# Kernel optimization log

Measured on AMD Instinct MI355X. Metric: run time of the kernel, lower is better.

The kernel has to match this reference:

```python
import jax, jax.numpy as jnp
import numpy as np

N_NODES = 100000
N_EDGES = 1600000
IN_C, HID_C, OUT_C = 128, 128, 64


def gcn_conv(x, src, dst, ew, W, b, n_nodes):
    """PyG GCNConv: symmetric-normalized aggregation with added self-loops.

    out = D^{-1/2} (A + I) D^{-1/2} (x @ W) + b,  D = deg(A+I)
    """
    h = x @ W  # [N, C_out]
    # degree at target nodes, including self-loop weight of 1
    deg = jax.ops.segment_sum(ew, dst, num_segments=n_nodes) + 1.0  # [N]
    dinv = jnp.where(deg > 0, jax.lax.rsqrt(deg), 0.0)
    norm = dinv[src] * ew * dinv[dst]  # [E]
    # gather-scale-scatter over edges + self-loop term (norm_ii = 1/deg_i)
    agg = jax.ops.segment_sum(h[src] * norm[:, None], dst, num_segments=n_nodes)
    agg = agg + h * (dinv * dinv)[:, None]
    return agg + b


def setup_inputs() -> dict:
    key = jax.random.key(0)
    ks = jax.random.split(key, 7)
    x = jax.random.normal(ks[0], (N_NODES, IN_C), dtype=jnp.float32)
    edge_index = jax.random.randint(ks[1], (2, N_EDGES), 0, N_NODES, dtype=jnp.int32)
    edge_weight = jax.random.uniform(ks[2], (N_EDGES,), dtype=jnp.float32)
    W1 = jax.random.normal(ks[3], (IN_C, HID_C), dtype=jnp.float32) / np.sqrt(IN_C)
    b1 = jnp.zeros((HID_C,), dtype=jnp.float32)
    W2 = jax.random.normal(ks[4], (HID_C, OUT_C), dtype=jnp.float32) / np.sqrt(HID_C)
    b2 = jnp.zeros((OUT_C,), dtype=jnp.float32)
    return {"x": x, "edge_index": edge_index, "edge_weight": edge_weight,
            "W1": W1, "b1": b1, "W2": W2, "b2": b2}


def reference(x, edge_index, edge_weight, W1, b1, W2, b2):
    src, dst = edge_index[0], edge_index[1]
    n = x.shape[0]
    h = gcn_conv(x, src, dst, edge_weight, W1, b1, n)
    h = jax.nn.relu(h)
    out = gcn_conv(h, src, dst, edge_weight, W2, b2, n)
    return out
```

## Files before the change

### kernel.cpp

```cpp
#include <hip/hip_runtime.h>


#define N_NODES 100000
#define CHUNK   2048
#define NBUCK   196
#define BSHIFT  9
#define BNODES  512
#define CAP     10240

typedef __attribute__((ext_vector_type(8))) short bf16x8;
typedef __attribute__((ext_vector_type(4))) float f32x4;

__device__ __forceinline__ unsigned bf16r(float f) {
    unsigned u = __float_as_uint(f);
    return (u + 0x7fffu + ((u >> 16) & 1u)) >> 16;
}
__device__ __forceinline__ float bf_lo(unsigned u) { return __uint_as_float(u << 16); }
__device__ __forceinline__ float bf_hi(unsigned u) { return __uint_as_float(u & 0xffff0000u); }

__device__ __forceinline__ void fma8(float* a, uint4 u, float w) {
    a[0] = fmaf(bf_lo(u.x), w, a[0]); a[1] = fmaf(bf_hi(u.x), w, a[1]);
    a[2] = fmaf(bf_lo(u.y), w, a[2]); a[3] = fmaf(bf_hi(u.y), w, a[3]);
    a[4] = fmaf(bf_lo(u.z), w, a[4]); a[5] = fmaf(bf_hi(u.z), w, a[5]);
    a[6] = fmaf(bf_lo(u.w), w, a[6]); a[7] = fmaf(bf_hi(u.w), w, a[7]);
}


__global__ __launch_bounds__(256) void a2F_kernel(
    const int* __restrict__ src, const int* __restrict__ dst,
    const float* __restrict__ ew, const float* __restrict__ W1,
    const float* __restrict__ W2, unsigned* __restrict__ Wt1,
    unsigned* __restrict__ Wt2, int* __restrict__ bucketCur,
    uint2* __restrict__ csrTmp, int E)
{
    __shared__ int hist[256], sc[256], exc[256], lcur[256], basel[256];
    __shared__ uint2 ent[CHUNK];
    __shared__ unsigned short bof[CHUNK];

    int t = threadIdx.x;
    if (blockIdx.x == 0) {
        for (int f = t; f < 128 * 64; f += 256) {
            int c = f % 128, j = f / 128;
            Wt1[c * 64 + j] = bf16r(W1[(size_t)(2 * j) * 128 + c]) |
                              (bf16r(W1[(size_t)(2 * j + 1) * 128 + c]) << 16);
        }
        return;
    }
    if (blockIdx.x == 1) {
        for (int f = t; f < 64 * 64; f += 256) {
            int c = f % 64, j = f / 64;
            Wt2[c * 64 + j] = bf16r(W2[(size_t)(2 * j) * 64 + c]) |
                              (bf16r(W2[(size_t)(2 * j + 1) * 64 + c]) << 16);
        }
        return;
    }
    int blk = blockIdx.x - 2;
    hist[t] = 0; lcur[t] = 0;
    __syncthreads();

    int e0 = blk * CHUNK;
    int nv = min(CHUNK, E - e0);
    int dv[CHUNK / 256]; int sv[CHUNK / 256]; unsigned wv[CHUNK / 256];
#pragma unroll
    for (int j = 0; j < CHUNK / 256; ++j) {
        int idx = t + j * 256;
        if (idx < nv) {
            int e = e0 + idx;
            dv[j] = dst[e]; sv[j] = src[e]; wv[j] = __float_as_uint(ew[e]);
            atomicAdd(&hist[dv[j] >> BSHIFT], 1);
        } else dv[j] = -1;
    }
    __syncthreads();
    int hv = hist[t];
    sc[t] = hv;
    __syncthreads();
#pragma unroll
    for (int off = 1; off < 256; off <<= 1) {
        int a = (t >= off) ? sc[t - off] : 0;
        __syncthreads();
        sc[t] += a;
        __syncthreads();
    }
    exc[t] = sc[t] - hv;
    basel[t] = (hv > 0) ? atomicAdd(&bucketCur[t], hv) : 0;
    __syncthreads();
#pragma unroll
    for (int j = 0; j < CHUNK / 256; ++j) {
        if (dv[j] >= 0) {
            int b  = dv[j] >> BSHIFT;
            int dl = dv[j] & (BNODES - 1);
            int p  = exc[b] + atomicAdd(&lcur[b], 1);
            ent[p] = make_uint2(((unsigned)dl << 17) | (unsigned)sv[j], wv[j]);
            bof[p] = (unsigned short)b;
        }
    }
    __syncthreads();
#pragma unroll
    for (int j = 0; j < CHUNK / 256; ++j) {
        int i = t + j * 256;
        if (i < nv) {
            int b = bof[i];
            csrTmp[(size_t)b * CAP + basel[b] + (i - exc[b])] = ent[i];
        }
    }
}


__global__ __launch_bounds__(1024) void bucketB_kernel(
    const uint2* __restrict__ csrTmp, const int* __restrict__ bucketSize,
    float* __restrict__ dinv, uint2* __restrict__ nodeinfo,
    uint2* __restrict__ csrF, int N)
{
    __shared__ uint2 ent[CAP];
    __shared__ unsigned long long dc[BNODES];
    __shared__ int scn[BNODES], beg[BNODES], cur[BNODES];
    int b = blockIdx.x, t = threadIdx.x;
    if (t < BNODES) { dc[t] = 0ull; cur[t] = 0; }
    __syncthreads();

    int sz = min(bucketSize[b], CAP);
    const uint2* reg = csrTmp + (size_t)b * CAP;
    for (int i = t; i < sz; i += 1024) {
        uint2 en = reg[i];
        ent[i] = en;
        int dl = (int)(en.x >> 17);
        unsigned fx = (unsigned)__float2uint_rn(__uint_as_float(en.y) * 16777216.0f);
        atomicAdd(&dc[dl], (1ull << 32) | (unsigned long long)fx);
    }
    __syncthreads();

    int cnt = 0; float dv = 1.0f;
    if (t < BNODES) {
        unsigned long long v = dc[t];
        cnt = (int)(v >> 32);
        dv = rsqrtf((float)(unsigned)(v & 0xffffffffull) * (1.0f / 16777216.0f) + 1.0f);
        scn[t] = cnt;
    }
    __syncthreads();
#pragma unroll
    for (int off = 1; off < BNODES; off <<= 1) {
        int a = 0;
        if (t < BNODES && t >= off) a = scn[t - off];
        __syncthreads();
        if (t < BNODES) scn[t] += a;
        __syncthreads();
    }
    if (t < BNODES) {
        int excl = scn[t] - cnt;
        beg[t] = excl;
        int gn = b * BNODES + t;
        if (gn < N) {
            dinv[gn] = dv;
            nodeinfo[gn] = make_uint2((unsigned)(b * CAP + excl), (unsigned)cnt);
        }
    }
    __syncthreads();

    uint2* outreg = csrF + (size_t)b * CAP;
    for (int i = t; i < sz; i += 1024) {
        uint2 en = ent[i];
        int dl = (int)(en.x >> 17);
        int p  = beg[dl] + atomicAdd(&cur[dl], 1);
        outreg[p] = make_uint2(en.x & 0x1FFFFu, en.y);
    }
}


__global__ __launch_bounds__(256) void gemm1_kernel(
    const float* __restrict__ Xf, const unsigned* __restrict__ Wt,
    const float* __restrict__ dinv, unsigned* __restrict__ Hb, int M)
{
    constexpr int LW = 68, KU = 64;
    __shared__ unsigned sA[64 * LW];
    __shared__ unsigned sB[128 * LW];
    __shared__ float sD[64];
    const int t = threadIdx.x;
    const int rbase = blockIdx.x * 64;

    if (t < 64) sD[t] = (rbase + t < M) ? dinv[rbase + t] : 0.f;
    for (int f = t; f < 128 * 16; f += 256) {
        int c = f >> 4, qd = f & 15;
        *(uint4*)&sB[c * LW + qd * 4] = *(const uint4*)&Wt[c * KU + qd * 4];
    }
    for (int f = t; f < 64 * 32; f += 256) {
        int r = f >> 5, c4 = f & 31;
        int gr = rbase + r;
        float4 v = make_float4(0.f, 0.f, 0.f, 0.f);
        if (gr < M) v = *(const float4*)&Xf[(size_t)gr * 128 + c4 * 4];
        sA[r * LW + c4 * 2]     = bf16r(v.x) | (bf16r(v.y) << 16);
        sA[r * LW + c4 * 2 + 1] = bf16r(v.z) | (bf16r(v.w) << 16);
    }
    __syncthreads();

    const int wave = t >> 6, lane = t & 63;
    const int quad = lane >> 4, lr = lane & 15;
    const int n0 = wave * 32;

    f32x4 acc[4][2];
#pragma unroll
    for (int mi = 0; mi < 4; ++mi)
#pragma unroll
        for (int ni = 0; ni < 2; ++ni)
            acc[mi][ni] = (f32x4){0.f, 0.f, 0.f, 0.f};

#pragma unroll
    for (int ks = 0; ks < 4; ++ks) {
        int ko = ks * 16 + quad * 4;
        bf16x8 b0 = *(const bf16x8*)&sB[(n0 + lr) * LW + ko];
        bf16x8 b1 = *(const bf16x8*)&sB[(n0 + 16 + lr) * LW + ko];
#pragma unroll
        for (int mi = 0; mi < 4; ++mi) {
            bf16x8 a = *(const bf16x8*)&sA[(mi * 16 + lr) * LW + ko];
            acc[mi][0] = __builtin_amdgcn_mfma_f32_16x16x32_bf16(a, b0, acc[mi][0], 0, 0, 0);
            acc[mi][1] = __builtin_amdgcn_mfma_f32_16x16x32_bf16(a, b1, acc[mi][1], 0, 0, 0);
        }
    }
    __syncthreads();

    unsigned short* sO = (unsigned short*)sA;
#pragma unroll
    for (int mi = 0; mi < 4; ++mi)
#pragma unroll
        for (int ni = 0; ni < 2; ++ni)
#pragma unroll
            for (int r = 0; r < 4; ++r) {
                int row = mi * 16 + quad * 4 + r;
                sO[row * (2 * LW) + n0 + ni * 16 + lr] =
                    (unsigned short)bf16r(acc[mi][ni][r] * sD[row]);
            }
    __syncthreads();

    for (int f = t; f < 64 * 64; f += 256) {
        int row = f >> 6, cu = f & 63;
        int gr = rbase + row;
        if (gr < M) Hb[(size_t)gr * 64 + cu] = sA[row * LW + cu];
    }
}


__global__ __launch_bounds__(512, 4) void gg_kernel(
    const uint2* __restrict__ nodeinfo, const uint2* __restrict__ csr,
    const uint4* __restrict__ Hb4,
    const float* __restrict__ dinv, const float* __restrict__ bias,
    const unsigned* __restrict__ Wt2, unsigned* __restrict__ H2, int N)
{
    __shared__ __align__(16) unsigned sG[16 * 68];
    __shared__ __align__(16) float    sO[16 * 68];
    __shared__ float sDi[16];

    const int t = threadIdx.x, wave = t >> 6, lane = t & 63;
    const int q = lane >> 4, cg = lane & 15;
    const int nb = blockIdx.x * 16;
    if (t < 16) sDi[t] = dinv[nb + t];

    const int m0 = wave * 2, m1 = m0 + 1;
    const int n0 = nb + m0, n1 = nb + m1;

    float one0 = (q == 0) ? 1.f : 0.f;
    float acc0[8], acc1[8];
    {
        uint4 su = Hb4[(size_t)n0 * 16 + cg];
        uint4 sv = Hb4[(size_t)n1 * 16 + cg];
        acc0[0] = bf_lo(su.x) * one0; acc0[1] = bf_hi(su.x) * one0;
        acc0[2] = bf_lo(su.y) * one0; acc0[3] = bf_hi(su.y) * one0;
        acc0[4] = bf_lo(su.z) * one0; acc0[5] = bf_hi(su.z) * one0;
        acc0[6] = bf_lo(su.w) * one0; acc0[7] = bf_hi(su.w) * one0;
        acc1[0] = bf_lo(sv.x) * one0; acc1[1] = bf_hi(sv.x) * one0;
        acc1[2] = bf_lo(sv.y) * one0; acc1[3] = bf_hi(sv.y) * one0;
        acc1[4] = bf_lo(sv.z) * one0; acc1[5] = bf_hi(sv.z) * one0;
        acc1[6] = bf_lo(sv.w) * one0; acc1[7] = bf_hi(sv.w) * one0;
    }
    uint2 i0 = nodeinfo[n0], i1 = nodeinfo[n1];
    int j0 = (int)i0.x, e0v = j0 + (int)i0.y;
    int j1 = (int)i1.x, e1v = j1 + (int)i1.y;

    while (j0 < e0v || j1 < e1v) {
        int cs0 = 0, cs1 = 0; float cw0 = 0.f, cw1 = 0.f;
        if (j0 + lane < e0v) { uint2 p = csr[j0 + lane]; cs0 = (int)p.x; cw0 = __uint_as_float(p.y); }
        if (j1 + lane < e1v) { uint2 p = csr[j1 + lane]; cs1 = (int)p.x; cw1 = __uint_as_float(p.y); }
        int r0 = e0v - j0; int mm0 = r0 < 0 ? 0 : (r0 > 64 ? 64 : r0);
        int r1 = e1v - j1; int mm1 = r1 < 0 ? 0 : (r1 > 64 ? 64 : r1);
        int mmx = mm0 > mm1 ? mm0 : mm1;

        int   s0 = __shfl(cs0, q),  s1 = __shfl(cs1, q);
        float w0 = __shfl(cw0, q),  w1 = __shfl(cw1, q);
        uint4 u0 = Hb4[(size_t)s0 * 16 + cg];
        uint4 u1 = Hb4[(size_t)s1 * 16 + cg];

        for (int k = 0; k < mmx; k += 4) {
            uint4 u0n = u0, u1n = u1;
            float w0n = 0.f, w1n = 0.f;
            if (k + 4 < mmx) {
                int s0n = __shfl(cs0, k + 4 + q), s1n = __shfl(cs1, k + 4 + q);
                w0n = __shfl(cw0, k + 4 + q);     w1n = __shfl(cw1, k + 4 + q);
                u0n = Hb4[(size_t)s0n * 16 + cg];
                u1n = Hb4[(size_t)s1n * 16 + cg];
            }
            fma8(acc0, u0, w0);
            fma8(acc1, u1, w1);
            u0 = u0n; u1 = u1n; w0 = w0n; w1 = w1n;
        }
        j0 += 64; j1 += 64;
    }

#pragma unroll
    for (int v = 0; v < 8; ++v) {
        acc0[v] += __shfl_xor(acc0[v], 16);
        acc0[v] += __shfl_xor(acc0[v], 32);
        acc1[v] += __shfl_xor(acc1[v], 16);
        acc1[v] += __shfl_xor(acc1[v], 32);
    }
    if (q == 0) {
        int c = cg * 8;
        float di0 = dinv[n0];
        uint4 pk;
        pk.x = bf16r(fmaxf(acc0[0] * di0 + bias[c + 0], 0.f)) |
               (bf16r(fmaxf(acc0[1] * di0 + bias[c + 1], 0.f)) << 16);
        pk.y = bf16r(fmaxf(acc0[2] * di0 + bias[c + 2], 0.f)) |
               (bf16r(fmaxf(acc0[3] * di0 + bias[c + 3], 0.f)) << 16);
        pk.z = bf16r(fmaxf(acc0[4] * di0 + bias[c + 4], 0.f)) |
               (bf16r(fmaxf(acc0[5] * di0 + bias[c + 5], 0.f)) << 16);
        pk.w = bf16r(fmaxf(acc0[6] * di0 + bias[c + 6], 0.f)) |
               (bf16r(fmaxf(acc0[7] * di0 + bias[c + 7], 0.f)) << 16);
        *(uint4*)&sG[m0 * 68 + cg * 4] = pk;
        float di1 = dinv[n1];
        pk.x = bf16r(fmaxf(acc1[0] * di1 + bias[c + 0], 0.f)) |
               (bf16r(fmaxf(acc1[1] * di1 + bias[c + 1], 0.f)) << 16);
        pk.y = bf16r(fmaxf(acc1[2] * di1 + bias[c + 2], 0.f)) |
               (bf16r(fmaxf(acc1[3] * di1 + bias[c + 3], 0.f)) << 16);
        pk.z = bf16r(fmaxf(acc1[4] * di1 + bias[c + 4], 0.f)) |
               (bf16r(fmaxf(acc1[5] * di1 + bias[c + 5], 0.f)) << 16);
        pk.w = bf16r(fmaxf(acc1[6] * di1 + bias[c + 6], 0.f)) |
               (bf16r(fmaxf(acc1[7] * di1 + bias[c + 7], 0.f)) << 16);
        *(uint4*)&sG[m1 * 68 + cg * 4] = pk;
    }
    __syncthreads();

    if (wave < 4) {
        const int quad = lane >> 4, lr = lane & 15;
        const int nt0 = wave * 16;
        f32x4 accv = (f32x4){0.f, 0.f, 0.f, 0.f};
#pragma unroll
        for (int ks = 0; ks < 4; ++ks) {
            int ko = ks * 16 + quad * 4;
            bf16x8 av = *(const bf16x8*)&sG[lr * 68 + ko];
            bf16x8 bv = *(const bf16x8*)&Wt2[(nt0 + lr) * 64 + ko];
            accv = __builtin_amdgcn_mfma_f32_16x16x32_bf16(av, bv, accv, 0, 0, 0);
        }
#pragma unroll
        for (int r = 0; r < 4; ++r)
            sO[(quad * 4 + r) * 68 + nt0 + lr] = accv[r];
    }
    __syncthreads();

    if (t < 512) {
        int row = t >> 5, cu = t & 31;
        float sc = sDi[row];
        unsigned pk = bf16r(sO[row * 68 + 2 * cu] * sc) |
                      (bf16r(sO[row * 68 + 2 * cu + 1] * sc) << 16);
        H2[(size_t)(nb + row) * 32 + cu] = pk;
    }
}


__global__ __launch_bounds__(256, 4) void gather64_kernel(
    const uint2* __restrict__ nodeinfo, const uint2* __restrict__ csr,
    const uint4* __restrict__ Hb4,
    const float* __restrict__ dinv, const float* __restrict__ bias,
    float* __restrict__ OUT, int N)
{
    const int wave = threadIdx.x >> 6, lane = threadIdx.x & 63;
    const int n0 = blockIdx.x * 8 + wave * 2, n1 = n0 + 1;
    if (n0 >= N) return;
    const int q  = lane >> 3;
    const int cg = lane & 7;

    float one0 = (q == 0) ? 1.f : 0.f;
    float acc0[8], acc1[8];
    {
        uint4 su = Hb4[(size_t)n0 * 8 + cg];
        uint4 sv = Hb4[(size_t)n1 * 8 + cg];
        acc0[0] = bf_lo(su.x) * one0; acc0[1] = bf_hi(su.x) * one0;
        acc0[2] = bf_lo(su.y) * one0; acc0[3] = bf_hi(su.y) * one0;
        acc0[4] = bf_lo(su.z) * one0; acc0[5] = bf_hi(su.z) * one0;
        acc0[6] = bf_lo(su.w) * one0; acc0[7] = bf_hi(su.w) * one0;
        acc1[0] = bf_lo(sv.x) * one0; acc1[1] = bf_hi(sv.x) * one0;
        acc1[2] = bf_lo(sv.y) * one0; acc1[3] = bf_hi(sv.y) * one0;
        acc1[4] = bf_lo(sv.z) * one0; acc1[5] = bf_hi(sv.z) * one0;
        acc1[6] = bf_lo(sv.w) * one0; acc1[7] = bf_hi(sv.w) * one0;
    }

    uint2 i0 = nodeinfo[n0], i1 = nodeinfo[n1];
    int j0 = (int)i0.x, e0v = j0 + (int)i0.y;
    int j1 = (int)i1.x, e1v = j1 + (int)i1.y;

    while (j0 < e0v || j1 < e1v) {
        int cs0 = 0, cs1 = 0; float cw0 = 0.f, cw1 = 0.f;
        if (j0 + lane < e0v) { uint2 p = csr[j0 + lane]; cs0 = (int)p.x; cw0 = __uint_as_float(p.y); }
        if (j1 + lane < e1v) { uint2 p = csr[j1 + lane]; cs1 = (int)p.x; cw1 = __uint_as_float(p.y); }
        int r0 = e0v - j0; int mm0 = r0 < 0 ? 0 : (r0 > 64 ? 64 : r0);
        int r1 = e1v - j1; int mm1 = r1 < 0 ? 0 : (r1 > 64 ? 64 : r1);
        int mmx = mm0 > mm1 ? mm0 : mm1;

        int   s0 = __shfl(cs0, q),  s1 = __shfl(cs1, q);
        float w0 = __shfl(cw0, q),  w1 = __shfl(cw1, q);
        uint4 u0 = Hb4[(size_t)s0 * 8 + cg];
        uint4 u1 = Hb4[(size_t)s1 * 8 + cg];

        for (int k = 0; k < mmx; k += 8) {
            uint4 u0n = u0, u1n = u1;
            float w0n = 0.f, w1n = 0.f;
            if (k + 8 < mmx) {
                int s0n = __shfl(cs0, k + 8 + q), s1n = __shfl(cs1, k + 8 + q);
                w0n = __shfl(cw0, k + 8 + q);     w1n = __shfl(cw1, k + 8 + q);
                u0n = Hb4[(size_t)s0n * 8 + cg];
                u1n = Hb4[(size_t)s1n * 8 + cg];
            }
            fma8(acc0, u0, w0);
            fma8(acc1, u1, w1);
            u0 = u0n; u1 = u1n; w0 = w0n; w1 = w1n;
        }
        j0 += 64; j1 += 64;
    }

#pragma unroll
    for (int v = 0; v < 8; ++v) {
        acc0[v] += __shfl_xor(acc0[v], 8);
        acc0[v] += __shfl_xor(acc0[v], 16);
        acc0[v] += __shfl_xor(acc0[v], 32);
        acc1[v] += __shfl_xor(acc1[v], 8);
        acc1[v] += __shfl_xor(acc1[v], 16);
        acc1[v] += __shfl_xor(acc1[v], 32);
    }

    int c = cg * 8 + q;
    OUT[(size_t)n0 * 64 + c] = acc0[q] * dinv[n0] + bias[c];
    OUT[(size_t)n1 * 64 + c] = acc1[q] * dinv[n1] + bias[c];
}

static inline size_t align_up(size_t x) { return (x + 255) & ~size_t(255); }

extern "C" void kernel_launch(void* const* d_in, const int* in_sizes, int n_in,
                              void* d_out, int out_size, void* d_ws, size_t ws_size,
                              hipStream_t stream)
{
    const float* x  = (const float*)d_in[0];
    const int*   ei = (const int*)d_in[1];
    const float* ew = (const float*)d_in[2];
    const float* W1 = (const float*)d_in[3];
    const float* b1 = (const float*)d_in[4];
    const float* W2 = (const float*)d_in[5];
    const float* b2 = (const float*)d_in[6];
    float* out = (float*)d_out;

    const int N = N_NODES;
    const int E = in_sizes[2];
    const int* src = ei;
    const int* dst = ei + E;

    const int NBLK = (E + CHUNK - 1) / CHUNK;
    const size_t REGION = (size_t)NBUCK * CAP;

    char* ws = (char*)d_ws;
    int*   bucketCur = (int*)ws;   ws += align_up((size_t)NBUCK * 4);
    float* dinv      = (float*)ws; ws += align_up((size_t)N * 4);
    uint2* nodeinfo  = (uint2*)ws; ws += align_up((size_t)N * 8);
    uint2* csrTmp    = (uint2*)ws; ws += align_up(REGION * 8);
    uint2* csrF      = (uint2*)ws; ws += align_up(REGION * 8);
    unsigned* Wt1    = (unsigned*)ws; ws += align_up((size_t)128 * 64 * 4);
    unsigned* Wt2    = (unsigned*)ws; ws += align_up((size_t)64 * 64 * 4);
    unsigned* h1     = (unsigned*)ws; ws += align_up((size_t)N * 64 * 4);
    unsigned* h2     = (unsigned*)ws; ws += align_up((size_t)N * 32 * 4);

    hipMemsetAsync(bucketCur, 0, (size_t)NBUCK * 4, stream);
    a2F_kernel<<<NBLK + 2, 256, 0, stream>>>(src, dst, ew, W1, W2,
                                             Wt1, Wt2, bucketCur, csrTmp, E);
    bucketB_kernel<<<NBUCK, 1024, 0, stream>>>(csrTmp, bucketCur, dinv, nodeinfo, csrF, N);
    gemm1_kernel<<<(N + 63) / 64, 256, 0, stream>>>(x, Wt1, dinv, h1, N);
    gg_kernel<<<N / 16, 512, 0, stream>>>(nodeinfo, csrF, (const uint4*)h1,
                                          dinv, b1, Wt2, h2, N);
    gather64_kernel<<<(N + 7) / 8, 256, 0, stream>>>(
        nodeinfo, csrF, (const uint4*)h2, dinv, b2, out, N);
}
```

Baseline: 272.5 us.

## Map one node per wave in fused gather-GEMM kernel, 8 edges in flight

The fused layer-1 gather and layer-2 GEMM kernel now gives each wave one node instead of two. Each lane handles 16 channels via two 16-byte loads, with 8 edges processed in parallel per step instead of 4. Blocks cover 8 nodes, the unused MFMA rows are zero-padded in shared memory, and launch bounds now ask for more blocks per CU. This is meant to remove the lockstep waste of iterating to the larger degree of two paired nodes and to increase memory-level parallelism. In exchange, half of each 16-row MFMA tile is padding and there are more blocks and more shuffle-reduction steps.

```diff
diff --git a/kernel.cpp b/kernel.cpp
--- a/kernel.cpp
+++ b/kernel.cpp
@@ -238,7 +238,7 @@
 }
 
 
-__global__ __launch_bounds__(512, 4) void gg_kernel(
+__global__ __launch_bounds__(512, 8) void gg_kernel(
     const uint2* __restrict__ nodeinfo, const uint2* __restrict__ csr,
     const uint4* __restrict__ Hb4,
     const float* __restrict__ dinv, const float* __restrict__ bias,
@@ -246,93 +246,86 @@
 {
     __shared__ __align__(16) unsigned sG[16 * 68];
     __shared__ __align__(16) float    sO[16 * 68];
-    __shared__ float sDi[16];
+    __shared__ float sDi[8];
 
     const int t = threadIdx.x, wave = t >> 6, lane = t & 63;
-    const int q = lane >> 4, cg = lane & 15;
-    const int nb = blockIdx.x * 16;
-    if (t < 16) sDi[t] = dinv[nb + t];
-
-    const int m0 = wave * 2, m1 = m0 + 1;
-    const int n0 = nb + m0, n1 = nb + m1;
+    const int q = lane >> 3, cg = lane & 7;
+    const int nb = blockIdx.x * 8;
+    const int node = nb + wave;
+    if (t < 8) sDi[t] = dinv[nb + t];
+    for (int f = t; f < 8 * 68; f += 512) sG[8 * 68 + f] = 0;
 
     float one0 = (q == 0) ? 1.f : 0.f;
-    float acc0[8], acc1[8];
+    float acc[16];
     {
-        uint4 su = Hb4[(size_t)n0 * 16 + cg];
-        uint4 sv = Hb4[(size_t)n1 * 16 + cg];
-        acc0[0] = bf_lo(su.x) * one0; acc0[1] = bf_hi(su.x) * one0;
-        acc0[2] = bf_lo(su.y) * one0; acc0[3] = bf_hi(su.y) * one0;
-        acc0[4] = bf_lo(su.z) * one0; acc0[5] = bf_hi(su.z) * one0;
-        acc0[6] = bf_lo(su.w) * one0; acc0[7] = bf_hi(su.w) * one0;
-        acc1[0] = bf_lo(sv.x) * one0; acc1[1] = bf_hi(sv.x) * one0;
-        acc1[2] = bf_lo(sv.y) * one0; acc1[3] = bf_hi(sv.y) * one0;
-        acc1[4] = bf_lo(sv.z) * one0; acc1[5] = bf_hi(sv.z) * one0;
-        acc1[6] = bf_lo(sv.w) * one0; acc1[7] = bf_hi(sv.w) * one0;
-    }
-    uint2 i0 = nodeinfo[n0], i1 = nodeinfo[n1];
-    int j0 = (int)i0.x, e0v = j0 + (int)i0.y;
-    int j1 = (int)i1.x, e1v = j1 + (int)i1.y;
-
-    while (j0 < e0v || j1 < e1v) {
-        int cs0 = 0, cs1 = 0; float cw0 = 0.f, cw1 = 0.f;
-        if (j0 + lane < e0v) { uint2 p = csr[j0 + lane]; cs0 = (int)p.x; cw0 = __uint_as_float(p.y); }
-        if (j1 + lane < e1v) { uint2 p = csr[j1 + lane]; cs1 = (int)p.x; cw1 = __uint_as_float(p.y); }
-        int r0 = e0v - j0; int mm0 = r0 < 0 ? 0 : (r0 > 64 ? 64 : r0);
-        int r1 = e1v - j1; int mm1 = r1 < 0 ? 0 : (r1 > 64 ? 64 : r1);
-        int mmx = mm0 > mm1 ? mm0 : mm1;
-
-        int   s0 = __shfl(cs0, q),  s1 = __shfl(cs1, q);
-        float w0 = __shfl(cw0, q),  w1 = __shfl(cw1, q);
-        uint4 u0 = Hb4[(size_t)s0 * 16 + cg];
-        uint4 u1 = Hb4[(size_t)s1 * 16 + cg];
-
-        for (int k = 0; k < mmx; k += 4) {
+        uint4 sa = Hb4[(size_t)node * 16 + cg * 2];
+        uint4 sb = Hb4[(size_t)node * 16 + cg * 2 + 1];
+        acc[0]  = bf_lo(sa.x) * one0; acc[1]  = bf_hi(sa.x) * one0;
+        acc[2]  = bf_lo(sa.y) * one0; acc[3]  = bf_hi(sa.y) * one0;
+        acc[4]  = bf_lo(sa.z) * one0; acc[5]  = bf_hi(sa.z) * one0;
+        acc[6]  = bf_lo(sa.w) * one0; acc[7]  = bf_hi(sa.w) * one0;
+        acc[8]  = bf_lo(sb.x) * one0; acc[9]  = bf_hi(sb.x) * one0;
+        acc[10] = bf_lo(sb.y) * one0; acc[11] = bf_hi(sb.y) * one0;
+        acc[12] = bf_lo(sb.z) * one0; acc[13] = bf_hi(sb.z) * one0;
+        acc[14] = bf_lo(sb.w) * one0; acc[15] = bf_hi(sb.w) * one0;
+    }
+    uint2 inf = nodeinfo[node];
+    int j = (int)inf.x, end = j + (int)inf.y;
+
+    while (j < end) {
+        int cs = 0; float cw = 0.f;
+        if (j + lane < end) { uint2 p = csr[j + lane]; cs = (int)p.x; cw = __uint_as_float(p.y); }
+        int rem = end - j; int mm = rem > 64 ? 64 : rem;
+
+        int   s = __shfl(cs, q);
+        float w = __shfl(cw, q);
+        uint4 u0 = Hb4[(size_t)s * 16 + cg * 2];
+        uint4 u1 = Hb4[(size_t)s * 16 + cg * 2 + 1];
+
+        for (int k = 0; k < mm; k += 8) {
             uint4 u0n = u0, u1n = u1;
-            float w0n = 0.f, w1n = 0.f;
-            if (k + 4 < mmx) {
-                int s0n = __shfl(cs0, k + 4 + q), s1n = __shfl(cs1, k + 4 + q);
-                w0n = __shfl(cw0, k + 4 + q);     w1n = __shfl(cw1, k + 4 + q);
-                u0n = Hb4[(size_t)s0n * 16 + cg];
-                u1n = Hb4[(size_t)s1n * 16 + cg];
+            float wn = 0.f;
+            if (k + 8 < mm) {
+                int sn = __shfl(cs, k + 8 + q);
+                wn = __shfl(cw, k + 8 + q);
+                u0n = Hb4[(size_t)sn * 16 + cg * 2];
+                u1n = Hb4[(size_t)sn * 16 + cg * 2 + 1];
             }
-            fma8(acc0, u0, w0);
-            fma8(acc1, u1, w1);
-            u0 = u0n; u1 = u1n; w0 = w0n; w1 = w1n;
-        }
-        j0 += 64; j1 += 64;
-    }
-
-#pragma unroll
-    for (int v = 0; v < 8; ++v) {
-        acc0[v] += __shfl_xor(acc0[v], 16);
-        acc0[v] += __shfl_xor(acc0[v], 32);
-        acc1[v] += __shfl_xor(acc1[v], 16);
-        acc1[v] += __shfl_xor(acc1[v], 32);
+            fma8(acc,     u0, w);
+            fma8(acc + 8, u1, w);
+            u0 = u0n; u1 = u1n; w = wn;
+        }
+        j += 64;
+    }
+
+#pragma unroll
+    for (int v = 0; v < 16; ++v) {
+        acc[v] += __shfl_xor(acc[v], 8);
+        acc[v] += __shfl_xor(acc[v], 16);
+        acc[v] += __shfl_xor(acc[v], 32);
     }
     if (q == 0) {
-        int c = cg * 8;
-        float di0 = dinv[n0];
+        float di = dinv[node];
+        int c = cg * 16;
         uint4 pk;
-        pk.x = bf16r(fmaxf(acc0[0] * di0 + bias[c + 0], 0.f)) |
-               (bf16r(fmaxf(acc0[1] * di0 + bias[c + 1], 0.f)) << 16);
-        pk.y = bf16r(fmaxf(acc0[2] * di0 + bias[c + 2], 0.f)) |
-               (bf16r(fmaxf(acc0[3] * di0 + bias[c + 3], 0.f)) << 16);
-        pk.z = bf16r(fmaxf(acc0[4] * di0 + bias[c + 4], 0.f)) |
-               (bf16r(fmaxf(acc0[5] * di0 + bias[c + 5], 0.f)) << 16);
-        pk.w = bf16r(fmaxf(acc0[6] * di0 + bias[c + 6], 0.f)) |
-               (bf16r(fmaxf(acc0[7] * di0 + bias[c + 7], 0.f)) << 16);
-        *(uint4*)&sG[m0 * 68 + cg * 4] = pk;
-        float di1 = dinv[n1];
-        pk.x = bf16r(fmaxf(acc1[0] * di1 + bias[c + 0], 0.f)) |
-               (bf16r(fmaxf(acc1[1] * di1 + bias[c + 1], 0.f)) << 16);
-        pk.y = bf16r(fmaxf(acc1[2] * di1 + bias[c + 2], 0.f)) |
-               (bf16r(fmaxf(acc1[3] * di1 + bias[c + 3], 0.f)) << 16);
-        pk.z = bf16r(fmaxf(acc1[4] * di1 + bias[c + 4], 0.f)) |
-               (bf16r(fmaxf(acc1[5] * di1 + bias[c + 5], 0.f)) << 16);
-        pk.w = bf16r(fmaxf(acc1[6] * di1 + bias[c + 6], 0.f)) |
-               (bf16r(fmaxf(acc1[7] * di1 + bias[c + 7], 0.f)) << 16);
-        *(uint4*)&sG[m1 * 68 + cg * 4] = pk;
+        pk.x = bf16r(fmaxf(acc[0]  * di + bias[c + 0], 0.f)) |
+               (bf16r(fmaxf(acc[1]  * di + bias[c + 1], 0.f)) << 16);
+        pk.y = bf16r(fmaxf(acc[2]  * di + bias[c + 2], 0.f)) |
+               (bf16r(fmaxf(acc[3]  * di + bias[c + 3], 0.f)) << 16);
+        pk.z = bf16r(fmaxf(acc[4]  * di + bias[c + 4], 0.f)) |
+               (bf16r(fmaxf(acc[5]  * di + bias[c + 5], 0.f)) << 16);
+        pk.w = bf16r(fmaxf(acc[6]  * di + bias[c + 6], 0.f)) |
+               (bf16r(fmaxf(acc[7]  * di + bias[c + 7], 0.f)) << 16);
+        *(uint4*)&sG[wave * 68 + cg * 8] = pk;
+        pk.x = bf16r(fmaxf(acc[8]  * di + bias[c + 8],  0.f)) |
+               (bf16r(fmaxf(acc[9]  * di + bias[c + 9],  0.f)) << 16);
+        pk.y = bf16r(fmaxf(acc[10] * di + bias[c + 10], 0.f)) |
+               (bf16r(fmaxf(acc[11] * di + bias[c + 11], 0.f)) << 16);
+        pk.z = bf16r(fmaxf(acc[12] * di + bias[c + 12], 0.f)) |
+               (bf16r(fmaxf(acc[13] * di + bias[c + 13], 0.f)) << 16);
+        pk.w = bf16r(fmaxf(acc[14] * di + bias[c + 14], 0.f)) |
+               (bf16r(fmaxf(acc[15] * di + bias[c + 15], 0.f)) << 16);
+        *(uint4*)&sG[wave * 68 + cg * 8 + 4] = pk;
     }
     __syncthreads();
 
@@ -353,7 +346,7 @@
     }
     __syncthreads();
 
-    if (t < 512) {
+    if (t < 256) {
         int row = t >> 5, cu = t & 31;
         float sc = sDi[row];
         unsigned pk = bf16r(sO[row * 68 + 2 * cu] * sc) |
@@ -477,8 +470,8 @@
                                              Wt1, Wt2, bucketCur, csrTmp, E);
     bucketB_kernel<<<NBUCK, 1024, 0, stream>>>(csrTmp, bucketCur, dinv, nodeinfo, csrF, N);
     gemm1_kernel<<<(N + 63) / 64, 256, 0, stream>>>(x, Wt1, dinv, h1, N);
-    gg_kernel<<<N / 16, 512, 0, stream>>>(nodeinfo, csrF, (const uint4*)h1,
-                                          dinv, b1, Wt2, h2, N);
+    gg_kernel<<<N / 8, 512, 0, stream>>>(nodeinfo, csrF, (const uint4*)h1,
+                                         dinv, b1, Wt2, h2, N);
     gather64_kernel<<<(N + 7) / 8, 256, 0, stream>>>(
         nodeinfo, csrF, (const uint4*)h2, dinv, b2, out, N);
 }
```

Result: slower. 293.4 us (+7.7%).
